# Kernel optimization log

Measured on AMD Instinct MI355X. Metric: run time of the kernel, lower is better.

Reference implementation:

```python
import jax, jax.numpy as jnp
import numpy as np

B, T, N, DIN = 16, 40, 64, 64
H = 256          # n_hid == msg_out == gru_hid (required by the module's own shape constraints)
MSG_HID = 256
DOUT = 64
E = N * (N - 1)  # fully-connected directed graph, no self loops


def _linear_params(key, fin, fout):
    kw, kb = jax.random.split(key)
    s = 1.0 / np.sqrt(fin)
    w = jax.random.uniform(kw, (fout, fin), minval=-s, maxval=s, dtype=jnp.float32)
    b = jax.random.uniform(kb, (fout,), minval=-s, maxval=s, dtype=jnp.float32)
    return w, b


def setup_inputs() -> dict:
    key = jax.random.key(0)
    ks = jax.random.split(key, 16)
    # one-hot incidence matrices for all ordered node pairs (i != j)
    pairs = np.array([(i, j) for i in range(N) for j in range(N) if i != j])
    eye = np.eye(N, dtype=np.float32)
    rel_send = jnp.asarray(eye[pairs[:, 0]])  # [E, N]
    rel_rec = jnp.asarray(eye[pairs[:, 1]])   # [E, N]

    inputs = jax.random.normal(ks[0], (B, T, N, DIN), dtype=jnp.float32)
    rel_types = jax.random.uniform(ks[1], (B, E, 2), dtype=jnp.float32)

    d = {"inputs": inputs, "rel_rec": rel_rec, "rel_send": rel_send, "rel_types": rel_types}
    names_dims = [
        ("msg_fc1", 2 * H, MSG_HID), ("msg_fc2", MSG_HID, H),
        ("gru_ir", DIN, H), ("gru_hr", H, H),
        ("gru_ii", DIN, H), ("gru_hi", H, H),
        ("gru_in", DIN, H), ("gru_hn", H, H),
        ("out_fc1", H, H), ("out_fc2", H, H), ("out_fc3", H, DOUT),
    ]
    for k, (name, fin, fout) in zip(ks[2:13], names_dims):
        w, b = _linear_params(k, fin, fout)
        d[name + "_w"] = w
        d[name + "_b"] = b
    return d


def _lin(x, w, b):
    return x @ w.T + b


def reference(inputs, rel_rec, rel_send, rel_types,
              msg_fc1_w, msg_fc1_b, msg_fc2_w, msg_fc2_b,
              gru_ir_w, gru_ir_b, gru_hr_w, gru_hr_b,
              gru_ii_w, gru_ii_b, gru_hi_w, gru_hi_b,
              gru_in_w, gru_in_b, gru_hn_w, gru_hn_b,
              out_fc1_w, out_fc1_b, out_fc2_w, out_fc2_b, out_fc3_w, out_fc3_b):
    b, t, n, _ = inputs.shape
    # both edge-type branches share the same message MLP, so the summed
    # message equals msg * (rel_types[...,0] + rel_types[...,1])
    type_sum = rel_types[:, :, 0:1] + rel_types[:, :, 1:2]  # [B, E, 1]

    def step(hidden, xt):
        # node2edge on hidden: [B, E, 2H]
        senders = jnp.einsum('en,bnh->beh', rel_send, hidden)
        receivers = jnp.einsum('en,bnh->beh', rel_rec, hidden)
        pre_msg = jnp.concatenate([senders, receivers], axis=-1)
        msg = jax.nn.relu(_lin(pre_msg, msg_fc1_w, msg_fc1_b))
        msg = jax.nn.relu(_lin(msg, msg_fc2_w, msg_fc2_b))
        all_msgs = msg * type_sum                                   # [B, E, H]
        agg_msgs = jnp.einsum('beh,en->bnh', all_msgs, rel_rec)     # edge2node
        r = jax.nn.sigmoid(_lin(xt, gru_ir_w, gru_ir_b) + _lin(agg_msgs, gru_hr_w, gru_hr_b))
        i = jax.nn.sigmoid(_lin(xt, gru_ii_w, gru_ii_b) + _lin(agg_msgs, gru_hi_w, gru_hi_b))
        nn_ = jnp.tanh(_lin(xt, gru_in_w, gru_in_b) + r * _lin(agg_msgs, gru_hn_w, gru_hn_b))
        hidden = (1.0 - i) * nn_ + i * hidden
        pred = jax.nn.relu(_lin(hidden, out_fc1_w, out_fc1_b))
        pred = jax.nn.relu(_lin(pred, out_fc2_w, out_fc2_b))
        pred = _lin(pred, out_fc3_w, out_fc3_b)
        return hidden, pred

    xs = jnp.transpose(inputs[:, :-1], (1, 0, 2, 3))  # time-major [T-1, B, N, DIN]
    h0 = jnp.zeros((b, n, H), dtype=inputs.dtype)
    _, preds = jax.lax.scan(step, h0, xs)
    return jnp.transpose(preds, (1, 0, 2, 3))          # [B, T-1, N, n_out]
```

## Files before the change

### kernel.cpp

```cpp
#include <hip/hip_runtime.h>
#include <math.h>


namespace {
constexpr int kB = 16, kT = 40, kTS = 39, kN = 64, kDin = 64, kH = 256;
constexpr int kE = kN * (kN - 1);
constexpr int kBN = kB * kN;
constexpr int kDout = 64;
}

typedef _Float16 half8 __attribute__((ext_vector_type(8)));
typedef float f32x4 __attribute__((ext_vector_type(4)));

__device__ __forceinline__ float sigm(float x) { return 1.f / (1.f + expf(-x)); }

__device__ __forceinline__ unsigned short f2h(float x) {
    _Float16 h = (_Float16)x;
    return __builtin_bit_cast(unsigned short, h);
}

__device__ __forceinline__ uint4 pack8h(const float* x) {
    unsigned us[8];
    #pragma unroll
    for (int q = 0; q < 8; ++q) us[q] = f2h(x[q]);
    uint4 p;
    p.x = us[0] | (us[1] << 16); p.y = us[2] | (us[3] << 16);
    p.z = us[4] | (us[5] << 16); p.w = us[6] | (us[7] << 16);
    return p;
}

__global__ void setup_kernel(
    const float* __restrict__ rel_rec, const float* __restrict__ rel_send,
    const float* __restrict__ rel_types, const float* __restrict__ W2,
    const float* __restrict__ Whr, const float* __restrict__ Whi,
    const float* __restrict__ Whn, const float* __restrict__ Wir,
    const float* __restrict__ Wii, const float* __restrict__ Win,
    const float* __restrict__ W1,
    const float* __restrict__ bir, const float* __restrict__ bhr,
    const float* __restrict__ bii, const float* __restrict__ bhi,
    const float* __restrict__ fc1w, const float* __restrict__ fc2w,
    const float* __restrict__ fc3w,
    int* __restrict__ edge_at, float* __restrict__ ts,
    unsigned short* __restrict__ W2f,
    unsigned short* __restrict__ Wri,
    unsigned short* __restrict__ Wnh,
    unsigned short* __restrict__ Wnx,
    unsigned short* __restrict__ Wuv,
    unsigned short* __restrict__ F1, unsigned short* __restrict__ F2,
    unsigned short* __restrict__ F3,
    float* __restrict__ bri) {
    int idx = blockIdx.x * 256 + threadIdx.x;
    if (idx < kE) {
        int si = 0, ri = 0;
        for (int n = 0; n < kN; ++n) {
            if (rel_send[idx * kN + n] > 0.5f) si = n;
            if (rel_rec[idx * kN + n] > 0.5f) ri = n;
        }
        edge_at[ri * kN + si] = idx;
    }
    if (idx < kB * kE) ts[idx] = rel_types[2 * idx] + rel_types[2 * idx + 1];
    if (idx < kH * kH) {
        W2f[idx] = f2h(W2[idx]);
        Wnh[idx] = f2h(Whn[idx]);
        F1[idx] = f2h(fc1w[idx]);
        F2[idx] = f2h(fc2w[idx]);
    }
    if (idx < 512 * 320) {
        int row = idx / 320, k = idx - row * 320;
        float v;
        if (row < 256) v = (k < kH) ? Whr[row * kH + k] : Wir[row * kDin + k - kH];
        else { int o = row - 256; v = (k < kH) ? Whi[o * kH + k] : Wii[o * kDin + k - kH]; }
        Wri[idx] = f2h(v);
    }
    if (idx < kH * kDin) Wnx[idx] = f2h(Win[idx]);
    if (idx < 512 * 256) {
        int row = idx >> 8, k = idx & 255;
        float v = (row < 256) ? W1[row * 512 + k] : W1[(row - 256) * 512 + 256 + k];
        Wuv[idx] = f2h(v);
    }
    if (idx < kDout * kH) F3[idx] = f2h(fc3w[idx]);
    if (idx < 256) bri[idx] = bir[idx] + bhr[idx];
    else if (idx < 512) bri[idx] = bii[idx - 256] + bhi[idx - 256];
}

__global__ __launch_bounds__(512, 2)
void step_kernel(const float* __restrict__ hprev,
                 const float* __restrict__ inputs, int t,
                 const float* __restrict__ Uin, const float* __restrict__ Vin,
                 const unsigned short* __restrict__ W2f,
                 const float* __restrict__ b1, const float* __restrict__ b2,
                 const float* __restrict__ ts, const int* __restrict__ edge_at,
                 const unsigned short* __restrict__ Wri,
                 const unsigned short* __restrict__ Wnh,
                 const unsigned short* __restrict__ Wnx,
                 const unsigned short* __restrict__ Wuv,
                 const float* __restrict__ bri, const float* __restrict__ bhn,
                 const float* __restrict__ bin_,
                 float* __restrict__ hnew,
                 float* __restrict__ Uo, float* __restrict__ Vo) {
    __shared__ __align__(16) unsigned short h1[kN * kH];
    __shared__ float vjb[kH];
    __shared__ float tssL[kN];
    __shared__ float aggL[4][kH];
    __shared__ __align__(16) unsigned short Zf[16 * 320];
    __shared__ __align__(16) unsigned short Hf[16 * 256];

    const int tid = threadIdx.x;
    const int lane = tid & 63, w = tid >> 6;
    const int mrow = lane & 15, mq = lane >> 4;
    const int m0 = blockIdx.x * 4;
    const int b = blockIdx.x >> 4, j0 = (blockIdx.x & 15) * 4;

    const unsigned short* Wp = W2f + (size_t)(w * 32 + mrow) * kH + mq * 8;
    half8 bb[8][2];
    #pragma unroll
    for (int kt = 0; kt < 8; ++kt)
        #pragma unroll
        for (int nf = 0; nf < 2; ++nf)
            bb[kt][nf] = *(const half8*)(Wp + nf * 16 * kH + kt * 32);
    __builtin_amdgcn_sched_barrier(0);

    #pragma unroll 1
    for (int jj = 0; jj < 4; ++jj) {
        const int j = j0 + jj;
        if (tid < kN) {
            int e = edge_at[j * kN + tid];
            tssL[tid] = (e < 0) ? 0.f : ts[b * kE + e];
        }
        if (tid < kH) vjb[tid] = Vin[(size_t)(b * kN + j) * kH + tid] + b1[tid];
        __syncthreads();

        {
            const int o = tid & 31, i0 = tid >> 5;
            const int k0 = o * 8;
            const float4 vj0 = *(const float4*)&vjb[k0];
            const float4 vj1 = *(const float4*)&vjb[k0 + 4];
            #pragma unroll
            for (int p = 0; p < 4; ++p) {
                const int i = i0 + 16 * p;
                const float4* up = (const float4*)(Uin + (size_t)(b * kN + i) * kH + k0);
                float4 f0 = up[0], f1 = up[1];
                float x[8] = {f0.x + vj0.x, f0.y + vj0.y, f0.z + vj0.z, f0.w + vj0.w,
                              f1.x + vj1.x, f1.y + vj1.y, f1.z + vj1.z, f1.w + vj1.w};
                #pragma unroll
                for (int q = 0; q < 8; ++q) x[q] = (i == j) ? 0.f : fmaxf(x[q], 0.f);
                const int byte = i * 512 + ((k0 * 2) ^ ((i & 7) << 4));
                *(uint4*)((char*)h1 + byte) = pack8h(x);
            }
        }
        __syncthreads();

        f32x4 acc[4][2];
        #pragma unroll
        for (int mf = 0; mf < 4; ++mf)
            #pragma unroll
            for (int nf = 0; nf < 2; ++nf) acc[mf][nf] = (f32x4){0.f, 0.f, 0.f, 0.f};
        #pragma unroll
        for (int kt = 0; kt < 8; ++kt) {
            const int k0 = kt * 32;
            half8 a[4];
            #pragma unroll
            for (int mf = 0; mf < 4; ++mf) {
                const int r = mf * 16 + mrow;
                const int byte = r * 512 + (((k0 + mq * 8) * 2) ^ ((r & 7) << 4));
                a[mf] = *(const half8*)((const char*)h1 + byte);
            }
            #pragma unroll
            for (int mf = 0; mf < 4; ++mf)
                #pragma unroll
                for (int nf = 0; nf < 2; ++nf)
                    acc[mf][nf] = __builtin_amdgcn_mfma_f32_16x16x32_f16(
                        a[mf], bb[kt][nf], acc[mf][nf], 0, 0, 0);
        }

        float tsr[16];
        #pragma unroll
        for (int mf = 0; mf < 4; ++mf)
            #pragma unroll
            for (int r = 0; r < 4; ++r)
                tsr[mf * 4 + r] = tssL[mf * 16 + mq * 4 + r];
        #pragma unroll
        for (int nf = 0; nf < 2; ++nf) {
            const int col = w * 32 + nf * 16 + mrow;
            const float bv = b2[col];
            float s = 0.f;
            #pragma unroll
            for (int mf = 0; mf < 4; ++mf)
                #pragma unroll
                for (int r = 0; r < 4; ++r)
                    s += tsr[mf * 4 + r] * fmaxf(acc[mf][nf][r] + bv, 0.f);
            s += __shfl_xor(s, 16);
            s += __shfl_xor(s, 32);
            if (lane < 16) aggL[jj][col] = s;
        }
        __syncthreads();
    }

    {
        const uint4 z4 = {0u, 0u, 0u, 0u};
        for (int c = tid; c < 4 * 40; c += 512) {
            const int r = c / 40, g = c - r * 40;
            float x[8];
            if (g < 32) {
                #pragma unroll
                for (int q = 0; q < 8; ++q) x[q] = aggL[r][g * 8 + q];
            } else {
                const int grow = m0 + r, bb_ = grow >> 6, n = grow & 63;
                const float* xp = inputs + ((size_t)(bb_ * kT + t) * kN + n) * kDin + (g - 32) * 8;
                *(float4*)&x[0] = ((const float4*)xp)[0];
                *(float4*)&x[4] = ((const float4*)xp)[1];
            }
            const int byte = r * 640 + ((g ^ (r & 7)) << 4);
            *(uint4*)((char*)Zf + byte) = pack8h(x);
        }
        for (int c = tid; c < 12 * 40; c += 512) {
            const int r = 4 + c / 40, g = c - (c / 40) * 40;
            const int byte = r * 640 + ((g ^ (r & 7)) << 4);
            *(uint4*)((char*)Zf + byte) = z4;
        }
        for (int c = tid; c < 12 * 32; c += 512) {
            const int r = 4 + c / 32, g = c & 31;
            const int byte = r * 512 + ((g ^ (r & 7)) << 4);
            *(uint4*)((char*)Hf + byte) = z4;
        }
    }
    __syncthreads();

    #pragma unroll
    for (int nf = 0; nf < 2; ++nf) {
        const int col = w * 32 + nf * 16 + mrow;
        const unsigned short* WR = Wri + (size_t)col * 320 + mq * 8;
        const unsigned short* WI = Wri + (size_t)(256 + col) * 320 + mq * 8;
        const unsigned short* WNh = Wnh + (size_t)col * kH + mq * 8;
        const unsigned short* WNx = Wnx + (size_t)col * kDin + mq * 8;

        half8 rwa[10][3];
        #pragma unroll
        for (int kt = 0; kt < 10; ++kt) {
            rwa[kt][0] = *(const half8*)(WR + kt * 32);
            rwa[kt][1] = *(const half8*)(WI + kt * 32);
            if (kt < 8) rwa[kt][2] = *(const half8*)(WNh + kt * 32);
            else        rwa[kt][2] = *(const half8*)(WNx + (kt * 32 - 256));
        }
        __builtin_amdgcn_sched_barrier(0);

        f32x4 aR = {0.f,0.f,0.f,0.f}, aI = {0.f,0.f,0.f,0.f};
        f32x4 aNH = {0.f,0.f,0.f,0.f}, aNX = {0.f,0.f,0.f,0.f};
        #pragma unroll
        for (int kt = 0; kt < 10; ++kt) {
            const int g = kt * 4 + mq;
            const int byte = mrow * 640 + ((g ^ (mrow & 7)) << 4);
            half8 zf = *(const half8*)((const char*)Zf + byte);
            aR = __builtin_amdgcn_mfma_f32_16x16x32_f16(zf, rwa[kt][0], aR, 0, 0, 0);
            aI = __builtin_amdgcn_mfma_f32_16x16x32_f16(zf, rwa[kt][1], aI, 0, 0, 0);
            if (kt < 8) aNH = __builtin_amdgcn_mfma_f32_16x16x32_f16(zf, rwa[kt][2], aNH, 0, 0, 0);
            else        aNX = __builtin_amdgcn_mfma_f32_16x16x32_f16(zf, rwa[kt][2], aNX, 0, 0, 0);
        }

        if (mq == 0) {
            const float brv = bri[col], biv = bri[256 + col];
            const float bhnv = bhn[col], binv = bin_[col];
            #pragma unroll
            for (int reg = 0; reg < 4; ++reg) {
                const int lr = reg;
                const int grow = m0 + lr;
                float rg = sigm(aR[reg] + brv);
                float ig = sigm(aI[reg] + biv);
                float ng = tanhf(aNX[reg] + binv + rg * (aNH[reg] + bhnv));
                float h2 = (1.f - ig) * ng + ig * hprev[(size_t)grow * kH + col];
                hnew[(size_t)grow * kH + col] = h2;
                const int byte = lr * 512 + (((col >> 3) ^ (lr & 7)) << 4) + (col & 7) * 2;
                *(unsigned short*)((char*)Hf + byte) = f2h(h2);
            }
        }
    }
    __syncthreads();

    #pragma unroll
    for (int nf = 0; nf < 4; ++nf) {
        const int col = w * 64 + nf * 16 + mrow;
        const unsigned short* Wp2 = Wuv + (size_t)col * kH + mq * 8;
        half8 rwa[8];
        #pragma unroll
        for (int kt = 0; kt < 8; ++kt) rwa[kt] = *(const half8*)(Wp2 + kt * 32);
        __builtin_amdgcn_sched_barrier(0);
        f32x4 aUV = {0.f, 0.f, 0.f, 0.f};
        #pragma unroll
        for (int kt = 0; kt < 8; ++kt) {
            const int g = kt * 4 + mq;
            const int byte = mrow * 512 + ((g ^ (mrow & 7)) << 4);
            half8 zf = *(const half8*)((const char*)Hf + byte);
            aUV = __builtin_amdgcn_mfma_f32_16x16x32_f16(zf, rwa[kt], aUV, 0, 0, 0);
        }
        if (mq == 0) {
            #pragma unroll
            for (int reg = 0; reg < 4; ++reg) {
                const int grow = m0 + reg;
                const float v = aUV[reg];
                if (col < 256) Uo[(size_t)grow * kH + col] = v;
                else Vo[(size_t)grow * kH + col - 256] = v;
            }
        }
    }
}

__global__ __launch_bounds__(256, 2)
void out_kernel(const float* __restrict__ hist,
                const unsigned short* __restrict__ F1,
                const unsigned short* __restrict__ F2,
                const unsigned short* __restrict__ F3,
                const float* __restrict__ fc1b, const float* __restrict__ fc2b,
                const float* __restrict__ fc3b, float* __restrict__ out) {
    __shared__ __align__(16) unsigned short Af[64 * 256];
    __shared__ __align__(16) unsigned short Bf[64 * 256];
    const int m0 = blockIdx.x * 64;
    const int tid = threadIdx.x;
    const int lane = tid & 63, w = tid >> 6;
    const int mrow = lane & 15, mq = lane >> 4;

    #pragma unroll
    for (int it = 0; it < 8; ++it) {
        const int c = tid + it * 256;
        const int r = c >> 5, o = c & 31;
        const float* ap = hist + (size_t)(m0 + r) * kH + o * 8;
        float x[8];
        *(float4*)&x[0] = ((const float4*)ap)[0];
        *(float4*)&x[4] = ((const float4*)ap)[1];
        const int byte = r * 512 + ((o << 4) ^ ((r & 7) << 4));
        *(uint4*)((char*)Af + byte) = pack8h(x);
    }
    __syncthreads();

    #define LAYER(SRC, WW, BIAS, DST)                                           \
    {                                                                           \
        const unsigned short* wb = WW + (size_t)(w * 64 + mrow) * kH + mq * 8;  \
        half8 wall[8][4];                                                       \
        _Pragma("unroll")                                                       \
        for (int kt = 0; kt < 8; ++kt)                                          \
            _Pragma("unroll")                                                   \
            for (int nf = 0; nf < 4; ++nf)                                      \
                wall[kt][nf] = *(const half8*)(wb + nf * 16 * kH + kt * 32);    \
        __builtin_amdgcn_sched_barrier(0);                                      \
        f32x4 acc[4][4];                                                        \
        _Pragma("unroll")                                                       \
        for (int m = 0; m < 4; ++m)                                             \
            _Pragma("unroll")                                                   \
            for (int nf = 0; nf < 4; ++nf) acc[m][nf] = (f32x4){0.f,0.f,0.f,0.f};\
        _Pragma("unroll")                                                       \
        for (int kt = 0; kt < 8; ++kt) {                                        \
            const int k0 = kt * 32;                                             \
            half8 zf[4];                                                        \
            _Pragma("unroll")                                                   \
            for (int m = 0; m < 4; ++m) {                                       \
                const int r = m * 16 + mrow;                                    \
                const int byte = r * 512 + (((k0 + mq * 8) * 2) ^ ((r & 7) << 4)); \
                zf[m] = *(const half8*)((const char*)SRC + byte);               \
            }                                                                   \
            _Pragma("unroll")                                                   \
            for (int m = 0; m < 4; ++m)                                         \
                _Pragma("unroll")                                               \
                for (int nf = 0; nf < 4; ++nf)                                  \
                    acc[m][nf] = __builtin_amdgcn_mfma_f32_16x16x32_f16(        \
                        zf[m], wall[kt][nf], acc[m][nf], 0, 0, 0);              \
        }                                                                       \
        _Pragma("unroll")                                                       \
        for (int m = 0; m < 4; ++m)                                             \
            _Pragma("unroll")                                                   \
            for (int nf = 0; nf < 4; ++nf) {                                    \
                const int col = w * 64 + nf * 16 + mrow;                        \
                const float bv = BIAS[col];                                     \
                _Pragma("unroll")                                               \
                for (int reg = 0; reg < 4; ++reg) {                             \
                    const int lr = m * 16 + mq * 4 + reg;                       \
                    float v = fmaxf(acc[m][nf][reg] + bv, 0.f);                 \
                    const int byte = lr * 512 + (((col >> 3) ^ (lr & 7)) << 4) + (col & 7) * 2; \
                    *(unsigned short*)((char*)DST + byte) = f2h(v);             \
                }                                                               \
            }                                                                   \
        __syncthreads();                                                        \
    }

    LAYER(Af, F1, fc1b, Bf)
    LAYER(Bf, F2, fc2b, Af)

    {
        const int row = w * 16 + mrow;
        const unsigned short* wb = F3 + (size_t)row * kH + mq * 8;
        half8 wall[8];
        #pragma unroll
        for (int kt = 0; kt < 8; ++kt) wall[kt] = *(const half8*)(wb + kt * 32);
        __builtin_amdgcn_sched_barrier(0);
        f32x4 acc[4];
        #pragma unroll
        for (int m = 0; m < 4; ++m) acc[m] = (f32x4){0.f, 0.f, 0.f, 0.f};
        #pragma unroll
        for (int kt = 0; kt < 8; ++kt) {
            const int k0 = kt * 32;
            half8 zf[4];
            #pragma unroll
            for (int m = 0; m < 4; ++m) {
                const int r = m * 16 + mrow;
                const int byte = r * 512 + (((k0 + mq * 8) * 2) ^ ((r & 7) << 4));
                zf[m] = *(const half8*)((const char*)Af + byte);
            }
            #pragma unroll
            for (int m = 0; m < 4; ++m)
                acc[m] = __builtin_amdgcn_mfma_f32_16x16x32_f16(zf[m], wall[kt], acc[m], 0, 0, 0);
        }
        const int col = w * 16 + mrow;
        const float bv = fc3b[col];
        #pragma unroll
        for (int m = 0; m < 4; ++m)
            #pragma unroll
            for (int reg = 0; reg < 4; ++reg) {
                const int grow = m0 + m * 16 + mq * 4 + reg;
                const int t = grow >> 10, bn = grow & 1023, b = bn >> 6, n = bn & 63;
                out[(((size_t)b * kTS + t) * kN + n) * kDout + col] = acc[m][reg] + bv;
            }
    }
    #undef LAYER
}

extern "C" void kernel_launch(void* const* d_in, const int* in_sizes, int n_in,
                              void* d_out, int out_size, void* d_ws, size_t ws_size,
                              hipStream_t stream) {
    const float* inputs    = (const float*)d_in[0];
    const float* rel_rec   = (const float*)d_in[1];
    const float* rel_send  = (const float*)d_in[2];
    const float* rel_types = (const float*)d_in[3];
    const float* W1  = (const float*)d_in[4];  const float* b1  = (const float*)d_in[5];
    const float* W2  = (const float*)d_in[6];  const float* b2  = (const float*)d_in[7];
    const float* Wir = (const float*)d_in[8];  const float* bir = (const float*)d_in[9];
    const float* Whr = (const float*)d_in[10]; const float* bhr = (const float*)d_in[11];
    const float* Wii = (const float*)d_in[12]; const float* bii = (const float*)d_in[13];
    const float* Whi = (const float*)d_in[14]; const float* bhi = (const float*)d_in[15];
    const float* Win = (const float*)d_in[16]; const float* bin_ = (const float*)d_in[17];
    const float* Whn = (const float*)d_in[18]; const float* bhn = (const float*)d_in[19];
    const float* fc1w = (const float*)d_in[20]; const float* fc1b = (const float*)d_in[21];
    const float* fc2w = (const float*)d_in[22]; const float* fc2b = (const float*)d_in[23];
    const float* fc3w = (const float*)d_in[24]; const float* fc3b = (const float*)d_in[25];
    float* out = (float*)d_out;

    char* w = (char*)d_ws;
    auto take = [&](size_t bytes) { char* p = w; w += (bytes + 255) & ~(size_t)255; return p; };
    int* edge_at = (int*)take(kN * kN * 4);
    float* ts = (float*)take(kB * kE * 4);
    unsigned short* W2f = (unsigned short*)take(kH * kH * 2);
    unsigned short* Wri = (unsigned short*)take(512 * 320 * 2);
    unsigned short* Wnh = (unsigned short*)take(kH * kH * 2);
    unsigned short* Wnx = (unsigned short*)take(kH * kDin * 2);
    unsigned short* Wuv = (unsigned short*)take(512 * 256 * 2);
    unsigned short* F1 = (unsigned short*)take(kH * kH * 2);
    unsigned short* F2 = (unsigned short*)take(kH * kH * 2);
    unsigned short* F3 = (unsigned short*)take(kDout * kH * 2);
    float* bri = (float*)take(512 * 4);
    float* Ua = (float*)take((size_t)kBN * kH * 4);
    float* Va = (float*)take((size_t)kBN * kH * 4);
    float* Ub = (float*)take((size_t)kBN * kH * 4);
    float* Vb = (float*)take((size_t)kBN * kH * 4);
    float* hh = (float*)w;

    hipMemsetAsync(edge_at, 0xFF, kN * kN * 4, stream);
    setup_kernel<<<640, 256, 0, stream>>>(
        rel_rec, rel_send, rel_types, W2, Whr, Whi, Whn, Wir, Wii, Win, W1,
        bir, bhr, bii, bhi, fc1w, fc2w, fc3w,
        edge_at, ts, W2f, Wri, Wnh, Wnx, Wuv, F1, F2, F3, bri);
    hipMemsetAsync(Ua, 0, (size_t)kBN * kH * 4, stream);
    hipMemsetAsync(Va, 0, (size_t)kBN * kH * 4, stream);
    hipMemsetAsync(hh, 0, (size_t)kBN * kH * 4, stream);

    float* Uc = Ua; float* Vc = Va; float* Un = Ub; float* Vn = Vb;
    for (int t = 0; t < kTS; ++t) {
        step_kernel<<<kBN / 4, 512, 0, stream>>>(
            hh + (size_t)t * kBN * kH, inputs, t, Uc, Vc,
            W2f, b1, b2, ts, edge_at, Wri, Wnh, Wnx, Wuv, bri, bhn, bin_,
            hh + (size_t)(t + 1) * kBN * kH, Un, Vn);
        float* tmp;
        tmp = Uc; Uc = Un; Un = tmp;
        tmp = Vc; Vc = Vn; Vn = tmp;
    }
    out_kernel<<<kTS * kBN / 64, 256, 0, stream>>>(
        hh + (size_t)kBN * kH, F1, F2, F3, fc1b, fc2b, fc3b, out);
}
```

Measured before the change: 1.601 ms.

## Process two destination nodes per round and store fp16 hidden history for output MLP

The message stage of the step kernel now builds two edge-hidden tiles at once in a doubled LDS buffer. Each half of the block's waves computes a 64-column slice for one node, so the loop runs 2 rounds instead of 4 and has fewer barriers. The V/ts preloads for all four nodes are hoisted ahead of the loop. The hidden history is also written once as fp16 to a separate buffer, and the fp32 hidden state ping-pongs between two buffers, so the output kernel reads half the bytes with no conversion. The cost is twice the B-fragment registers (8x4 half8) and double the h1 LDS, which may reduce occupancy under launch_bounds(512,2).

```diff
diff --git a/kernel.cpp b/kernel.cpp
--- a/kernel.cpp
+++ b/kernel.cpp
@@ -10,6 +10,7 @@
 }
 
 typedef _Float16 half8 __attribute__((ext_vector_type(8)));
+typedef short short8 __attribute__((ext_vector_type(8)));
 typedef float f32x4 __attribute__((ext_vector_type(4)));
 
 __device__ __forceinline__ float sigm(float x) { return 1.f / (1.f + expf(-x)); }
@@ -97,10 +98,11 @@
                  const float* __restrict__ bri, const float* __restrict__ bhn,
                  const float* __restrict__ bin_,
                  float* __restrict__ hnew,
-                 float* __restrict__ Uo, float* __restrict__ Vo) {
-    __shared__ __align__(16) unsigned short h1[kN * kH];
-    __shared__ float vjb[kH];
-    __shared__ float tssL[kN];
+                 float* __restrict__ Uo, float* __restrict__ Vo,
+                 unsigned short* __restrict__ hist16) {
+    __shared__ __align__(16) unsigned short h1[2][kN * kH];
+    __shared__ float vjb4[4][kH];
+    __shared__ float tss4[4][kN];
     __shared__ float aggL[4][kH];
     __shared__ __align__(16) unsigned short Zf[16 * 320];
     __shared__ __align__(16) unsigned short Hf[16 * 256];
@@ -111,33 +113,42 @@
     const int m0 = blockIdx.x * 4;
     const int b = blockIdx.x >> 4, j0 = (blockIdx.x & 15) * 4;
 
-    const unsigned short* Wp = W2f + (size_t)(w * 32 + mrow) * kH + mq * 8;
-    half8 bb[8][2];
+    {
+        const int jj = tid >> 7, o = tid & 127;
+        const int j = j0 + jj;
+        vjb4[jj][o] = Vin[(size_t)(b * kN + j) * kH + o] + b1[o];
+        vjb4[jj][o + 128] = Vin[(size_t)(b * kN + j) * kH + o + 128] + b1[o + 128];
+        if (o < kN) {
+            int e = edge_at[j * kN + o];
+            tss4[jj][o] = (e < 0) ? 0.f : ts[b * kE + e];
+        }
+    }
+
+    const int wcol = w & 3;
+    const int wp = w >> 2;
+    const unsigned short* Wp = W2f + (size_t)(wcol * 64 + mrow) * kH + mq * 8;
+    half8 bb[8][4];
     #pragma unroll
     for (int kt = 0; kt < 8; ++kt)
         #pragma unroll
-        for (int nf = 0; nf < 2; ++nf)
+        for (int nf = 0; nf < 4; ++nf)
             bb[kt][nf] = *(const half8*)(Wp + nf * 16 * kH + kt * 32);
     __builtin_amdgcn_sched_barrier(0);
+    __syncthreads();
 
     #pragma unroll 1
-    for (int jj = 0; jj < 4; ++jj) {
-        const int j = j0 + jj;
-        if (tid < kN) {
-            int e = edge_at[j * kN + tid];
-            tssL[tid] = (e < 0) ? 0.f : ts[b * kE + e];
-        }
-        if (tid < kH) vjb[tid] = Vin[(size_t)(b * kN + j) * kH + tid] + b1[tid];
-        __syncthreads();
-
+    for (int round = 0; round < 2; ++round) {
         {
-            const int o = tid & 31, i0 = tid >> 5;
+            const int pb = tid >> 8, tl = tid & 255;
+            const int jj = round * 2 + pb;
+            const int j = j0 + jj;
+            const int o = tl & 31, i0 = tl >> 5;
             const int k0 = o * 8;
-            const float4 vj0 = *(const float4*)&vjb[k0];
-            const float4 vj1 = *(const float4*)&vjb[k0 + 4];
-            #pragma unroll
-            for (int p = 0; p < 4; ++p) {
-                const int i = i0 + 16 * p;
+            const float4 vj0 = *(const float4*)&vjb4[jj][k0];
+            const float4 vj1 = *(const float4*)&vjb4[jj][k0 + 4];
+            #pragma unroll
+            for (int p = 0; p < 8; ++p) {
+                const int i = i0 + 8 * p;
                 const float4* up = (const float4*)(Uin + (size_t)(b * kN + i) * kH + k0);
                 float4 f0 = up[0], f1 = up[1];
                 float x[8] = {f0.x + vj0.x, f0.y + vj0.y, f0.z + vj0.z, f0.w + vj0.w,
@@ -145,16 +156,17 @@
                 #pragma unroll
                 for (int q = 0; q < 8; ++q) x[q] = (i == j) ? 0.f : fmaxf(x[q], 0.f);
                 const int byte = i * 512 + ((k0 * 2) ^ ((i & 7) << 4));
-                *(uint4*)((char*)h1 + byte) = pack8h(x);
+                *(uint4*)((char*)h1[pb] + byte) = pack8h(x);
             }
         }
         __syncthreads();
 
-        f32x4 acc[4][2];
+        const int jj = round * 2 + wp;
+        f32x4 acc[4][4];
         #pragma unroll
         for (int mf = 0; mf < 4; ++mf)
             #pragma unroll
-            for (int nf = 0; nf < 2; ++nf) acc[mf][nf] = (f32x4){0.f, 0.f, 0.f, 0.f};
+            for (int nf = 0; nf < 4; ++nf) acc[mf][nf] = (f32x4){0.f, 0.f, 0.f, 0.f};
         #pragma unroll
         for (int kt = 0; kt < 8; ++kt) {
             const int k0 = kt * 32;
@@ -163,12 +175,12 @@
             for (int mf = 0; mf < 4; ++mf) {
                 const int r = mf * 16 + mrow;
                 const int byte = r * 512 + (((k0 + mq * 8) * 2) ^ ((r & 7) << 4));
-                a[mf] = *(const half8*)((const char*)h1 + byte);
+                a[mf] = *(const half8*)((const char*)h1[wp] + byte);
             }
             #pragma unroll
             for (int mf = 0; mf < 4; ++mf)
                 #pragma unroll
-                for (int nf = 0; nf < 2; ++nf)
+                for (int nf = 0; nf < 4; ++nf)
                     acc[mf][nf] = __builtin_amdgcn_mfma_f32_16x16x32_f16(
                         a[mf], bb[kt][nf], acc[mf][nf], 0, 0, 0);
         }
@@ -178,10 +190,10 @@
         for (int mf = 0; mf < 4; ++mf)
             #pragma unroll
             for (int r = 0; r < 4; ++r)
-                tsr[mf * 4 + r] = tssL[mf * 16 + mq * 4 + r];
-        #pragma unroll
-        for (int nf = 0; nf < 2; ++nf) {
-            const int col = w * 32 + nf * 16 + mrow;
+                tsr[mf * 4 + r] = tss4[jj][mf * 16 + mq * 4 + r];
+        #pragma unroll
+        for (int nf = 0; nf < 4; ++nf) {
+            const int col = wcol * 64 + nf * 16 + mrow;
             const float bv = b2[col];
             float s = 0.f;
             #pragma unroll
@@ -269,8 +281,10 @@
                 float ng = tanhf(aNX[reg] + binv + rg * (aNH[reg] + bhnv));
                 float h2 = (1.f - ig) * ng + ig * hprev[(size_t)grow * kH + col];
                 hnew[(size_t)grow * kH + col] = h2;
+                const unsigned short hv = f2h(h2);
+                hist16[((size_t)t * kBN + grow) * kH + col] = hv;
                 const int byte = lr * 512 + (((col >> 3) ^ (lr & 7)) << 4) + (col & 7) * 2;
-                *(unsigned short*)((char*)Hf + byte) = f2h(h2);
+                *(unsigned short*)((char*)Hf + byte) = hv;
             }
         }
     }
@@ -305,7 +319,7 @@
 }
 
 __global__ __launch_bounds__(256, 2)
-void out_kernel(const float* __restrict__ hist,
+void out_kernel(const unsigned short* __restrict__ hist16,
                 const unsigned short* __restrict__ F1,
                 const unsigned short* __restrict__ F2,
                 const unsigned short* __restrict__ F3,
@@ -322,12 +336,9 @@
     for (int it = 0; it < 8; ++it) {
         const int c = tid + it * 256;
         const int r = c >> 5, o = c & 31;
-        const float* ap = hist + (size_t)(m0 + r) * kH + o * 8;
-        float x[8];
-        *(float4*)&x[0] = ((const float4*)ap)[0];
-        *(float4*)&x[4] = ((const float4*)ap)[1];
+        short8 v = *(const short8*)(hist16 + (size_t)(m0 + r) * kH + o * 8);
         const int byte = r * 512 + ((o << 4) ^ ((r & 7) << 4));
-        *(uint4*)((char*)Af + byte) = pack8h(x);
+        *(short8*)((char*)Af + byte) = v;
     }
     __syncthreads();
 
@@ -458,7 +469,9 @@
     float* Va = (float*)take((size_t)kBN * kH * 4);
     float* Ub = (float*)take((size_t)kBN * kH * 4);
     float* Vb = (float*)take((size_t)kBN * kH * 4);
-    float* hh = (float*)w;
+    float* ha = (float*)take((size_t)kBN * kH * 4);
+    float* hb_ = (float*)take((size_t)kBN * kH * 4);
+    unsigned short* hist16 = (unsigned short*)take((size_t)kTS * kBN * kH * 2);
 
     hipMemsetAsync(edge_at, 0xFF, kN * kN * 4, stream);
     setup_kernel<<<640, 256, 0, stream>>>(
@@ -467,18 +480,20 @@
         edge_at, ts, W2f, Wri, Wnh, Wnx, Wuv, F1, F2, F3, bri);
     hipMemsetAsync(Ua, 0, (size_t)kBN * kH * 4, stream);
     hipMemsetAsync(Va, 0, (size_t)kBN * kH * 4, stream);
-    hipMemsetAsync(hh, 0, (size_t)kBN * kH * 4, stream);
+    hipMemsetAsync(ha, 0, (size_t)kBN * kH * 4, stream);
 
     float* Uc = Ua; float* Vc = Va; float* Un = Ub; float* Vn = Vb;
+    float* hc = ha; float* hn = hb_;
     for (int t = 0; t < kTS; ++t) {
         step_kernel<<<kBN / 4, 512, 0, stream>>>(
-            hh + (size_t)t * kBN * kH, inputs, t, Uc, Vc,
+            hc, inputs, t, Uc, Vc,
             W2f, b1, b2, ts, edge_at, Wri, Wnh, Wnx, Wuv, bri, bhn, bin_,
-            hh + (size_t)(t + 1) * kBN * kH, Un, Vn);
+            hn, Un, Vn, hist16);
         float* tmp;
         tmp = Uc; Uc = Un; Un = tmp;
         tmp = Vc; Vc = Vn; Vn = tmp;
+        tmp = hc; hc = hn; hn = tmp;
     }
     out_kernel<<<kTS * kBN / 64, 256, 0, stream>>>(
-        hh + (size_t)kBN * kH, F1, F2, F3, fc1b, fc2b, fc3b, out);
-}
+        hist16, F1, F2, F3, fc1b, fc2b, fc3b, out);
+}
```

New measurement: 2.456 ms. +53.4%, slower.
